# Optimization experiments

Measured on AMD Instinct MI355X. Metric: run time of the kernel, lower is better.

The kernel has to match this reference:

```python
import jax, jax.numpy as jnp
import numpy as np
from itertools import product

N = 120000      # active voxels
D = 128         # dense grid resolution per axis
CIN = 64
COUT = 64
K = 27          # 3x3x3 kernel volume
EPS = 1e-5


def setup_inputs() -> dict:
    # Build a random sparse voxel set and its kernel-offset neighbor map (torchsparse kmap).
    rng = np.random.default_rng(0)
    flat = rng.choice(D ** 3, size=N, replace=False)
    cz, cy, cx = np.unravel_index(flat, (D, D, D))
    coords = np.stack([cz, cy, cx], axis=1)               # [N, 3]
    lut = np.full(D ** 3, -1, dtype=np.int64)
    lut[flat] = np.arange(N)
    nbr = np.empty((K, N), dtype=np.int32)
    for k, (dz, dy, dx) in enumerate(product((-1, 0, 1), repeat=3)):
        nc = coords + np.array([dz, dy, dx])
        valid = np.all((nc >= 0) & (nc < D), axis=1)
        fl = np.ravel_multi_index(np.clip(nc, 0, D - 1).T, (D, D, D))
        nbr[k] = np.where(valid, lut[fl], -1).astype(np.int32)

    key = jax.random.key(0)
    k1, k2, k3, k4 = jax.random.split(key, 4)
    feats = jax.random.normal(k1, (N, CIN), dtype=jnp.float32)
    # torchsparse Conv3d weight layout: [kernel_volume, in_channels, out_channels]
    weight = jax.random.normal(k2, (K, CIN, COUT), dtype=jnp.float32) / np.float32(np.sqrt(K * CIN))
    gamma = jax.random.uniform(k3, (COUT,), dtype=jnp.float32, minval=0.5, maxval=1.5)
    beta = jax.random.normal(k4, (COUT,), dtype=jnp.float32) * 0.1
    return {"feats": feats, "weight": weight, "gamma": gamma, "beta": beta,
            "neighbor_idx": jnp.asarray(nbr)}


def reference(feats, weight, gamma, beta, neighbor_idx):
    # Sparse conv = gather -> per-offset matmul -> accumulate (stride 1, same voxel set).
    mask = (neighbor_idx >= 0)                      # [K, N]
    safe = jnp.maximum(neighbor_idx, 0)
    gathered = feats[safe] * mask[..., None]        # [K, N, Cin], missing neighbors zeroed
    out = jnp.einsum('knc,kcd->nd', gathered, weight)  # [N, Cout]
    # BatchNorm over active voxels (training-mode batch statistics), then ReLU.
    mean = out.mean(axis=0)
    var = out.var(axis=0)
    y = gamma * (out - mean) * jax.lax.rsqrt(var + EPS) + beta
    return jnp.maximum(y, 0.0)
```

## Files before the change

### kernel.cpp

```cpp
#include <hip/hip_runtime.h>

#define NVOX 120000
#define KVOL 27
#define CH 64
#define TOTAL (NVOX * CH)
#define NF4 (TOTAL / 4)
#define EPSV 1e-5f

typedef __attribute__((ext_vector_type(8))) short bf16x8;
typedef __attribute__((ext_vector_type(8))) unsigned short u16x8;
typedef __attribute__((ext_vector_type(4))) float f32x4;
typedef __attribute__((address_space(1))) const void gconst_t;
typedef __attribute__((address_space(3))) void lvoid_t;

__device__ __forceinline__ unsigned short f2bf(float f) {
    unsigned int u = __builtin_bit_cast(unsigned int, f);
    u += 0x7FFFu + ((u >> 16) & 1u);
    return (unsigned short)(u >> 16);
}

#define PGRID (27 + 3750)
__global__ void prep(const float* __restrict__ w, const float* __restrict__ feats,
                     unsigned short* __restrict__ wtf, unsigned short* __restrict__ fb,
                     float* __restrict__ stats) {
    __shared__ unsigned short ls[4096];
    const int b = blockIdx.x;
    const int tid = threadIdx.x;
    if (b < KVOL) {
        const int k = b;
        float4 v[4];
        const float4* src = (const float4*)(w + (size_t)k * 4096 + tid * 16);
#pragma unroll
        for (int i = 0; i < 4; ++i) v[i] = src[i];
#pragma unroll
        for (int e = 0; e < 16; ++e) {
            const int t = tid * 16 + e;
            const int d = t & 63, c = t >> 6;
            const int grp = (d >> 4) * 2 + (c >> 5);
            const int l = ((c & 31) >> 3) * 16 + (d & 15);
            const int j = c & 7;
            ls[(grp * 64 + l) * 8 + j] = f2bf(((const float*)v)[e]);
        }
        __syncthreads();
        u16x8* dst = (u16x8*)(wtf + (size_t)k * 4096);
        const u16x8* lsv = (const u16x8*)ls;
        dst[tid * 2]     = lsv[tid * 2];
        dst[tid * 2 + 1] = lsv[tid * 2 + 1];
        if (b == 0 && tid < 128) stats[tid] = 0.f;
        if (b == 1 && tid < 8) ((u16x8*)fb)[(size_t)NVOX * 8 + tid] = (u16x8)0;
    } else {
        const int t = (b - KVOL) * 256 + tid;
        const float4* src = (const float4*)feats + (size_t)t * 2;
        const float4 p0 = src[0];
        const float4 p1 = src[1];
        u16x8 v = {f2bf(p0.x), f2bf(p0.y), f2bf(p0.z), f2bf(p0.w),
                   f2bf(p1.x), f2bf(p1.y), f2bf(p1.z), f2bf(p1.w)};
        ((u16x8*)fb)[t] = v;
    }
}

__launch_bounds__(256, 4)
__global__ void conv_mfma(const unsigned short* __restrict__ FB,
                          const unsigned short* __restrict__ WtF,
                          const int* __restrict__ nbr,
                          float* __restrict__ out,
                          float* __restrict__ stats) {
    __shared__ unsigned short wlds[2][4096];
    __shared__ float lstats[128];
    const int tid = threadIdx.x;
    const int lane = tid & 63;
    const int wv = tid >> 6;
    const int m = lane & 15;
    const int q = lane >> 4;
    const int v0 = blockIdx.x * 128 + wv * 32;
    const bool tv[2] = { v0 < NVOX, v0 + 16 < NVOX };
    const int r[2] = { v0 + m, v0 + 16 + m };

    f32x4 acc[2][4];
#pragma unroll
    for (int t = 0; t < 2; ++t)
#pragma unroll
        for (int nt = 0; nt < 4; ++nt)
            acc[t][nt] = (f32x4){0.f, 0.f, 0.f, 0.f};
    if (tid < 128) lstats[tid] = 0.f;

    const bf16x8* fbv = (const bf16x8*)FB;

    {
        const unsigned short* g = WtF + wv * 1024 + lane * 8;
        __builtin_amdgcn_global_load_lds((gconst_t*)g,         (lvoid_t*)&wlds[0][wv * 1024],       16, 0, 0);
        __builtin_amdgcn_global_load_lds((gconst_t*)(g + 512), (lvoid_t*)&wlds[0][wv * 1024 + 512], 16, 0, 0);
    }
    __builtin_amdgcn_sched_barrier(0);

    bf16x8 a[2][2];
    unsigned long long msk[2];
    int idxn[2];
#pragma unroll
    for (int t = 0; t < 2; ++t) {
        const int rr = tv[t] ? r[t] : m;
        const int i0 = nbr[rr];
        const int i = tv[t] ? i0 : -1;
        msk[t] = __ballot(i >= 0);
        const bf16x8* row = fbv + (size_t)(i < 0 ? NVOX : i) * 8;
        a[t][0] = row[q];
        a[t][1] = row[q + 4];
        const int i1 = nbr[NVOX + rr];
        idxn[t] = tv[t] ? i1 : -1;
    }
    asm volatile("s_waitcnt vmcnt(6) lgkmcnt(0)" ::: "memory");
    __builtin_amdgcn_s_barrier();
    __builtin_amdgcn_sched_barrier(0);

    for (int k = 0; k < KVOL; ++k) {
        const int nb = k & 1;
        if (k + 1 < KVOL) {
            const unsigned short* g = WtF + (size_t)(k + 1) * 4096 + wv * 1024 + lane * 8;
            __builtin_amdgcn_global_load_lds((gconst_t*)g,         (lvoid_t*)&wlds[nb ^ 1][wv * 1024],       16, 0, 0);
            __builtin_amdgcn_global_load_lds((gconst_t*)(g + 512), (lvoid_t*)&wlds[nb ^ 1][wv * 1024 + 512], 16, 0, 0);
        }
        __builtin_amdgcn_sched_barrier(0);

        unsigned long long mn[2];
        bf16x8 an[2][2];
#pragma unroll
        for (int t = 0; t < 2; ++t) {
            mn[t] = __ballot(idxn[t] >= 0);
            const bf16x8* rw = fbv + (size_t)(idxn[t] < 0 ? NVOX : idxn[t]) * 8;
            an[t][0] = rw[q];
            an[t][1] = rw[q + 4];
        }
        const int kk = (k + 2 < KVOL) ? (k + 2) : 0;
        const int* nbp = nbr + (size_t)kk * NVOX;
        int idxf[2];
#pragma unroll
        for (int t = 0; t < 2; ++t) {
            const int rr = tv[t] ? r[t] : m;
            const int v = nbp[rr];
            idxf[t] = (tv[t] && (k + 2 < KVOL)) ? v : -1;
        }

        const unsigned short* wk = &wlds[nb][lane * 8];
        bf16x8 bfr[8];
#pragma unroll
        for (int h = 0; h < 8; ++h)
            bfr[h] = *(const bf16x8*)(wk + h * 512);

#pragma unroll
        for (int t = 0; t < 2; ++t) {
            if (msk[t]) {
#pragma unroll
                for (int nt = 0; nt < 4; ++nt) {
                    acc[t][nt] = __builtin_amdgcn_mfma_f32_16x16x32_bf16(a[t][0], bfr[nt * 2 + 0], acc[t][nt], 0, 0, 0);
                    acc[t][nt] = __builtin_amdgcn_mfma_f32_16x16x32_bf16(a[t][1], bfr[nt * 2 + 1], acc[t][nt], 0, 0, 0);
                }
            }
        }

#pragma unroll
        for (int t = 0; t < 2; ++t) {
            a[t][0] = an[t][0];
            a[t][1] = an[t][1];
            msk[t] = mn[t];
            idxn[t] = idxf[t];
        }

        asm volatile("s_waitcnt vmcnt(6)" ::: "memory");
        __builtin_amdgcn_s_barrier();
        __builtin_amdgcn_sched_barrier(0);
    }

#pragma unroll
    for (int t = 0; t < 2; ++t) {
        if (tv[t]) {
            float* ob = out + (size_t)(v0 + t * 16 + q * 4) * CH + m;
#pragma unroll
            for (int nt = 0; nt < 4; ++nt)
#pragma unroll
                for (int rr = 0; rr < 4; ++rr)
                    ob[(size_t)rr * CH + nt * 16] = acc[t][nt][rr];
        }
    }

#pragma unroll
    for (int nt = 0; nt < 4; ++nt) {
        float s = 0.f, s2 = 0.f;
#pragma unroll
        for (int t = 0; t < 2; ++t)
#pragma unroll
            for (int rr = 0; rr < 4; ++rr) {
                const float x = acc[t][nt][rr];
                s += x;
                s2 = fmaf(x, x, s2);
            }
        s  += __shfl_xor(s, 16);  s  += __shfl_xor(s, 32);
        s2 += __shfl_xor(s2, 16); s2 += __shfl_xor(s2, 32);
        if (lane < 16) {
            atomicAdd(&lstats[nt * 16 + m], s);
            atomicAdd(&lstats[64 + nt * 16 + m], s2);
        }
    }
    __syncthreads();
    if (tid < 128) atomicAdd(&stats[tid], lstats[tid]);
}

__launch_bounds__(256)
__global__ void bn_relu(float* __restrict__ out, const float* __restrict__ stats,
                        const float* __restrict__ gamma, const float* __restrict__ beta) {
    __shared__ float sb[128];
    const int tid = threadIdx.x;
    if (tid < 64) {
        const float inv_n = 1.0f / (float)NVOX;
        const float mean = stats[tid] * inv_n;
        const float var = stats[64 + tid] * inv_n - mean * mean;
        const float sc = gamma[tid] * rsqrtf(var + EPSV);
        sb[tid] = sc;
        sb[64 + tid] = beta[tid] - mean * sc;
    }
    __syncthreads();
    float4* o4 = (float4*)out;
    const int base = blockIdx.x * 256 + tid;
    const int cb = (base & 15) * 4;
    const float s0 = sb[cb + 0], s1 = sb[cb + 1], s2 = sb[cb + 2], s3 = sb[cb + 3];
    const float b0 = sb[64 + cb + 0], b1 = sb[64 + cb + 1], b2 = sb[64 + cb + 2], b3 = sb[64 + cb + 3];
#pragma unroll
    for (int i = 0; i < 4; ++i) {
        const int e = base + i * 480000;
        float4 x = o4[e];
        x.x = fmaxf(fmaf(x.x, s0, b0), 0.f);
        x.y = fmaxf(fmaf(x.y, s1, b1), 0.f);
        x.z = fmaxf(fmaf(x.z, s2, b2), 0.f);
        x.w = fmaxf(fmaf(x.w, s3, b3), 0.f);
        o4[e] = x;
    }
}

extern "C" void kernel_launch(void* const* d_in, const int* in_sizes, int n_in,
                              void* d_out, int out_size, void* d_ws, size_t ws_size,
                              hipStream_t stream) {
    const float* feats  = (const float*)d_in[0];
    const float* weight = (const float*)d_in[1];
    const float* gamma  = (const float*)d_in[2];
    const float* beta   = (const float*)d_in[3];
    const int*   nbr    = (const int*)d_in[4];
    float* out = (float*)d_out;

    float* stats = (float*)d_ws;
    unsigned short* WtF = (unsigned short*)((char*)d_ws + 512);
    unsigned short* FB  = (unsigned short*)((char*)d_ws + 512 + 221184);

    prep<<<PGRID, 256, 0, stream>>>(weight, feats, WtF, FB, stats);
    conv_mfma<<<(NVOX + 127) / 128, 256, 0, stream>>>(FB, WtF, nbr, out, stats);
    bn_relu<<<1875, 256, 0, stream>>>(out, stats, gamma, beta);
}
```

Before: 154.2 us.

## Load weight fragments directly into registers and drop LDS staging and barriers

Weight fragments are no longer staged through double-buffered LDS with global_load_lds and per-offset block barriers. Each wave now reads its B fragments straight from global memory into registers, ping-ponging two register sets across a two-way unrolled loop. This removes the LDS traffic and block-wide synchronisation from the main loop. In exchange every wave issues its own weight loads, which should hit in L2, and register pressure rises, so launch bounds drop from 4 to 3 blocks per CU. A __syncthreads is added before the LDS stats reduction.

New measurement: 162.2 us. 5.2% more time.

```diff
diff --git a/kernel.cpp b/kernel.cpp
--- a/kernel.cpp
+++ b/kernel.cpp
@@ -10,8 +10,6 @@
 typedef __attribute__((ext_vector_type(8))) short bf16x8;
 typedef __attribute__((ext_vector_type(8))) unsigned short u16x8;
 typedef __attribute__((ext_vector_type(4))) float f32x4;
-typedef __attribute__((address_space(1))) const void gconst_t;
-typedef __attribute__((address_space(3))) void lvoid_t;
 
 __device__ __forceinline__ unsigned short f2bf(float f) {
     unsigned int u = __builtin_bit_cast(unsigned int, f);
@@ -59,13 +57,12 @@
     }
 }
 
-__launch_bounds__(256, 4)
+__launch_bounds__(256, 3)
 __global__ void conv_mfma(const unsigned short* __restrict__ FB,
                           const unsigned short* __restrict__ WtF,
                           const int* __restrict__ nbr,
                           float* __restrict__ out,
                           float* __restrict__ stats) {
-    __shared__ unsigned short wlds[2][4096];
     __shared__ float lstats[128];
     const int tid = threadIdx.x;
     const int lane = tid & 63;
@@ -85,89 +82,74 @@
     if (tid < 128) lstats[tid] = 0.f;
 
     const bf16x8* fbv = (const bf16x8*)FB;
-
-    {
-        const unsigned short* g = WtF + wv * 1024 + lane * 8;
-        __builtin_amdgcn_global_load_lds((gconst_t*)g,         (lvoid_t*)&wlds[0][wv * 1024],       16, 0, 0);
-        __builtin_amdgcn_global_load_lds((gconst_t*)(g + 512), (lvoid_t*)&wlds[0][wv * 1024 + 512], 16, 0, 0);
-    }
-    __builtin_amdgcn_sched_barrier(0);
-
-    bf16x8 a[2][2];
-    unsigned long long msk[2];
-    int idxn[2];
+    const bf16x8* wfr = (const bf16x8*)WtF + lane;
+
+    bf16x8 bfrA[8], bfrB[8];
+#pragma unroll
+    for (int h = 0; h < 8; ++h) bfrA[h] = wfr[h * 64];
+
+    bf16x8 aA[2][2], aB[2][2];
+    bool mskA[2], mskB[2];
+    int ixA[2], ixB[2];
 #pragma unroll
     for (int t = 0; t < 2; ++t) {
         const int rr = tv[t] ? r[t] : m;
         const int i0 = nbr[rr];
         const int i = tv[t] ? i0 : -1;
-        msk[t] = __ballot(i >= 0);
+        mskA[t] = (__ballot(i >= 0) != 0ULL);
         const bf16x8* row = fbv + (size_t)(i < 0 ? NVOX : i) * 8;
-        a[t][0] = row[q];
-        a[t][1] = row[q + 4];
+        aA[t][0] = row[q];
+        aA[t][1] = row[q + 4];
         const int i1 = nbr[NVOX + rr];
-        idxn[t] = tv[t] ? i1 : -1;
-    }
-    asm volatile("s_waitcnt vmcnt(6) lgkmcnt(0)" ::: "memory");
-    __builtin_amdgcn_s_barrier();
-    __builtin_amdgcn_sched_barrier(0);
-
-    for (int k = 0; k < KVOL; ++k) {
-        const int nb = k & 1;
-        if (k + 1 < KVOL) {
-            const unsigned short* g = WtF + (size_t)(k + 1) * 4096 + wv * 1024 + lane * 8;
-            __builtin_amdgcn_global_load_lds((gconst_t*)g,         (lvoid_t*)&wlds[nb ^ 1][wv * 1024],       16, 0, 0);
-            __builtin_amdgcn_global_load_lds((gconst_t*)(g + 512), (lvoid_t*)&wlds[nb ^ 1][wv * 1024 + 512], 16, 0, 0);
-        }
-        __builtin_amdgcn_sched_barrier(0);
-
-        unsigned long long mn[2];
-        bf16x8 an[2][2];
+        ixA[t] = tv[t] ? i1 : -1;
+    }
+
+    auto phase = [&](const bf16x8 (&bfrC)[8], bf16x8 (&bfrN)[8],
+                     const bf16x8 (&aC)[2][2], bf16x8 (&aN)[2][2],
+                     const bool (&mC)[2], bool (&mN)[2],
+                     const int (&ixC)[2], int (&ixN)[2], const int k) {
+#pragma unroll
+        for (int h = 0; h < 8; ++h) bfrN[h] = wfr[(k + 1) * 512 + h * 64];
 #pragma unroll
         for (int t = 0; t < 2; ++t) {
-            mn[t] = __ballot(idxn[t] >= 0);
-            const bf16x8* rw = fbv + (size_t)(idxn[t] < 0 ? NVOX : idxn[t]) * 8;
-            an[t][0] = rw[q];
-            an[t][1] = rw[q + 4];
+            mN[t] = (__ballot(ixC[t] >= 0) != 0ULL);
+            const bf16x8* rw = fbv + (size_t)(ixC[t] < 0 ? NVOX : ixC[t]) * 8;
+            aN[t][0] = rw[q];
+            aN[t][1] = rw[q + 4];
         }
         const int kk = (k + 2 < KVOL) ? (k + 2) : 0;
         const int* nbp = nbr + (size_t)kk * NVOX;
-        int idxf[2];
 #pragma unroll
         for (int t = 0; t < 2; ++t) {
             const int rr = tv[t] ? r[t] : m;
             const int v = nbp[rr];
-            idxf[t] = (tv[t] && (k + 2 < KVOL)) ? v : -1;
-        }
-
-        const unsigned short* wk = &wlds[nb][lane * 8];
-        bf16x8 bfr[8];
-#pragma unroll
-        for (int h = 0; h < 8; ++h)
-            bfr[h] = *(const bf16x8*)(wk + h * 512);
-
+            ixN[t] = (tv[t] && (k + 2 < KVOL)) ? v : -1;
+        }
 #pragma unroll
         for (int t = 0; t < 2; ++t) {
-            if (msk[t]) {
+            if (mC[t]) {
 #pragma unroll
                 for (int nt = 0; nt < 4; ++nt) {
-                    acc[t][nt] = __builtin_amdgcn_mfma_f32_16x16x32_bf16(a[t][0], bfr[nt * 2 + 0], acc[t][nt], 0, 0, 0);
-                    acc[t][nt] = __builtin_amdgcn_mfma_f32_16x16x32_bf16(a[t][1], bfr[nt * 2 + 1], acc[t][nt], 0, 0, 0);
+                    acc[t][nt] = __builtin_amdgcn_mfma_f32_16x16x32_bf16(aC[t][0], bfrC[nt * 2 + 0], acc[t][nt], 0, 0, 0);
+                    acc[t][nt] = __builtin_amdgcn_mfma_f32_16x16x32_bf16(aC[t][1], bfrC[nt * 2 + 1], acc[t][nt], 0, 0, 0);
                 }
             }
         }
-
-#pragma unroll
-        for (int t = 0; t < 2; ++t) {
-            a[t][0] = an[t][0];
-            a[t][1] = an[t][1];
-            msk[t] = mn[t];
-            idxn[t] = idxf[t];
-        }
-
-        asm volatile("s_waitcnt vmcnt(6)" ::: "memory");
-        __builtin_amdgcn_s_barrier();
-        __builtin_amdgcn_sched_barrier(0);
+    };
+
+    for (int k = 0; k < KVOL - 1; k += 2) {
+        phase(bfrA, bfrB, aA, aB, mskA, mskB, ixA, ixB, k);
+        phase(bfrB, bfrA, aB, aA, mskB, mskA, ixB, ixA, k + 1);
+    }
+#pragma unroll
+    for (int t = 0; t < 2; ++t) {
+        if (mskA[t]) {
+#pragma unroll
+            for (int nt = 0; nt < 4; ++nt) {
+                acc[t][nt] = __builtin_amdgcn_mfma_f32_16x16x32_bf16(aA[t][0], bfrA[nt * 2 + 0], acc[t][nt], 0, 0, 0);
+                acc[t][nt] = __builtin_amdgcn_mfma_f32_16x16x32_bf16(aA[t][1], bfrA[nt * 2 + 1], acc[t][nt], 0, 0, 0);
+            }
+        }
     }
 
 #pragma unroll
@@ -182,6 +164,7 @@
         }
     }
 
+    __syncthreads();
 #pragma unroll
     for (int nt = 0; nt < 4; ++nt) {
         float s = 0.f, s2 = 0.f;
```

## Gather fp32 features directly in conv and convert to bf16 in-register

Applied to the files above, without the earlier changes.

Removes the separate feature-to-bf16 conversion pass from the prep kernel, so the conv kernel gathers fp32 rows straight from the input and converts them to bf16 in registers before the MFMAs. This saves a full read and write of the feature array plus most of the prep launch. The cost is that each gather now moves twice as many bytes per neighbor across 27 offsets, and more registers are needed. Occupancy is lowered to 3 waves, and the software pipeline is rewritten as a ping-pong double-buffered lambda with a vmcnt of 10. The skip of all-invalid MFMA groups is also dropped in favor of zeroing invalid rows.

Result: slower. 184.0 us (+19.3%).

```diff
diff --git a/kernel.cpp b/kernel.cpp
--- a/kernel.cpp
+++ b/kernel.cpp
@@ -19,48 +19,34 @@
     return (unsigned short)(u >> 16);
 }
 
-#define PGRID (27 + 3750)
-__global__ void prep(const float* __restrict__ w, const float* __restrict__ feats,
-                     unsigned short* __restrict__ wtf, unsigned short* __restrict__ fb,
+__global__ void prep(const float* __restrict__ w, unsigned short* __restrict__ wtf,
                      float* __restrict__ stats) {
     __shared__ unsigned short ls[4096];
-    const int b = blockIdx.x;
+    const int k = blockIdx.x;
     const int tid = threadIdx.x;
-    if (b < KVOL) {
-        const int k = b;
-        float4 v[4];
-        const float4* src = (const float4*)(w + (size_t)k * 4096 + tid * 16);
-#pragma unroll
-        for (int i = 0; i < 4; ++i) v[i] = src[i];
-#pragma unroll
-        for (int e = 0; e < 16; ++e) {
-            const int t = tid * 16 + e;
-            const int d = t & 63, c = t >> 6;
-            const int grp = (d >> 4) * 2 + (c >> 5);
-            const int l = ((c & 31) >> 3) * 16 + (d & 15);
-            const int j = c & 7;
-            ls[(grp * 64 + l) * 8 + j] = f2bf(((const float*)v)[e]);
-        }
-        __syncthreads();
-        u16x8* dst = (u16x8*)(wtf + (size_t)k * 4096);
-        const u16x8* lsv = (const u16x8*)ls;
-        dst[tid * 2]     = lsv[tid * 2];
-        dst[tid * 2 + 1] = lsv[tid * 2 + 1];
-        if (b == 0 && tid < 128) stats[tid] = 0.f;
-        if (b == 1 && tid < 8) ((u16x8*)fb)[(size_t)NVOX * 8 + tid] = (u16x8)0;
-    } else {
-        const int t = (b - KVOL) * 256 + tid;
-        const float4* src = (const float4*)feats + (size_t)t * 2;
-        const float4 p0 = src[0];
-        const float4 p1 = src[1];
-        u16x8 v = {f2bf(p0.x), f2bf(p0.y), f2bf(p0.z), f2bf(p0.w),
-                   f2bf(p1.x), f2bf(p1.y), f2bf(p1.z), f2bf(p1.w)};
-        ((u16x8*)fb)[t] = v;
-    }
-}
-
-__launch_bounds__(256, 4)
-__global__ void conv_mfma(const unsigned short* __restrict__ FB,
+    float4 v[4];
+    const float4* src = (const float4*)(w + (size_t)k * 4096 + tid * 16);
+#pragma unroll
+    for (int i = 0; i < 4; ++i) v[i] = src[i];
+#pragma unroll
+    for (int e = 0; e < 16; ++e) {
+        const int t = tid * 16 + e;
+        const int d = t & 63, c = t >> 6;
+        const int grp = (d >> 4) * 2 + (c >> 5);
+        const int l = ((c & 31) >> 3) * 16 + (d & 15);
+        const int j = c & 7;
+        ls[(grp * 64 + l) * 8 + j] = f2bf(((const float*)v)[e]);
+    }
+    __syncthreads();
+    u16x8* dst = (u16x8*)(wtf + (size_t)k * 4096);
+    const u16x8* lsv = (const u16x8*)ls;
+    dst[tid * 2]     = lsv[tid * 2];
+    dst[tid * 2 + 1] = lsv[tid * 2 + 1];
+    if (k == 0 && tid < 128) stats[tid] = 0.f;
+}
+
+__launch_bounds__(256, 3)
+__global__ void conv_mfma(const float* __restrict__ feats,
                           const unsigned short* __restrict__ WtF,
                           const int* __restrict__ nbr,
                           float* __restrict__ out,
@@ -84,8 +70,6 @@
             acc[t][nt] = (f32x4){0.f, 0.f, 0.f, 0.f};
     if (tid < 128) lstats[tid] = 0.f;
 
-    const bf16x8* fbv = (const bf16x8*)FB;
-
     {
         const unsigned short* g = WtF + wv * 1024 + lane * 8;
         __builtin_amdgcn_global_load_lds((gconst_t*)g,         (lvoid_t*)&wlds[0][wv * 1024],       16, 0, 0);
@@ -93,26 +77,30 @@
     }
     __builtin_amdgcn_sched_barrier(0);
 
-    bf16x8 a[2][2];
-    unsigned long long msk[2];
-    int idxn[2];
+    float4 pA[2][4], pB[2][4];
+    bool invA[2], invB[2];
+    int ixA[2], ixB[2];
 #pragma unroll
     for (int t = 0; t < 2; ++t) {
         const int rr = tv[t] ? r[t] : m;
         const int i0 = nbr[rr];
-        const int i = tv[t] ? i0 : -1;
-        msk[t] = __ballot(i >= 0);
-        const bf16x8* row = fbv + (size_t)(i < 0 ? NVOX : i) * 8;
-        a[t][0] = row[q];
-        a[t][1] = row[q + 4];
+        const int ii = tv[t] ? i0 : -1;
+        invA[t] = (ii < 0);
+        const float* row = feats + (size_t)(ii < 0 ? 0 : ii) * CH + q * 8;
+        pA[t][0] = *(const float4*)(row);
+        pA[t][1] = *(const float4*)(row + 4);
+        pA[t][2] = *(const float4*)(row + 32);
+        pA[t][3] = *(const float4*)(row + 36);
         const int i1 = nbr[NVOX + rr];
-        idxn[t] = tv[t] ? i1 : -1;
-    }
-    asm volatile("s_waitcnt vmcnt(6) lgkmcnt(0)" ::: "memory");
+        ixA[t] = tv[t] ? i1 : -1;
+    }
+    asm volatile("s_waitcnt vmcnt(10) lgkmcnt(0)" ::: "memory");
     __builtin_amdgcn_s_barrier();
     __builtin_amdgcn_sched_barrier(0);
 
-    for (int k = 0; k < KVOL; ++k) {
+    auto phase = [&](const float4 (&pC)[2][4], float4 (&pN)[2][4],
+                     const bool (&invC)[2], bool (&invN)[2],
+                     const int (&ixC)[2], int (&ixN)[2], const int k) {
         const int nb = k & 1;
         if (k + 1 < KVOL) {
             const unsigned short* g = WtF + (size_t)(k + 1) * 4096 + wv * 1024 + lane * 8;
@@ -121,23 +109,23 @@
         }
         __builtin_amdgcn_sched_barrier(0);
 
-        unsigned long long mn[2];
-        bf16x8 an[2][2];
 #pragma unroll
         for (int t = 0; t < 2; ++t) {
-            mn[t] = __ballot(idxn[t] >= 0);
-            const bf16x8* rw = fbv + (size_t)(idxn[t] < 0 ? NVOX : idxn[t]) * 8;
-            an[t][0] = rw[q];
-            an[t][1] = rw[q + 4];
+            const int ii = ixC[t];
+            invN[t] = (ii < 0);
+            const float* row = feats + (size_t)(ii < 0 ? 0 : ii) * CH + q * 8;
+            pN[t][0] = *(const float4*)(row);
+            pN[t][1] = *(const float4*)(row + 4);
+            pN[t][2] = *(const float4*)(row + 32);
+            pN[t][3] = *(const float4*)(row + 36);
         }
         const int kk = (k + 2 < KVOL) ? (k + 2) : 0;
         const int* nbp = nbr + (size_t)kk * NVOX;
-        int idxf[2];
 #pragma unroll
         for (int t = 0; t < 2; ++t) {
             const int rr = tv[t] ? r[t] : m;
             const int v = nbp[rr];
-            idxf[t] = (tv[t] && (k + 2 < KVOL)) ? v : -1;
+            ixN[t] = (tv[t] && (k + 2 < KVOL)) ? v : -1;
         }
 
         const unsigned short* wk = &wlds[nb][lane * 8];
@@ -148,27 +136,32 @@
 
 #pragma unroll
         for (int t = 0; t < 2; ++t) {
-            if (msk[t]) {
-#pragma unroll
-                for (int nt = 0; nt < 4; ++nt) {
-                    acc[t][nt] = __builtin_amdgcn_mfma_f32_16x16x32_bf16(a[t][0], bfr[nt * 2 + 0], acc[t][nt], 0, 0, 0);
-                    acc[t][nt] = __builtin_amdgcn_mfma_f32_16x16x32_bf16(a[t][1], bfr[nt * 2 + 1], acc[t][nt], 0, 0, 0);
-                }
+            bf16x8 a0 = (bf16x8){(short)f2bf(pC[t][0].x), (short)f2bf(pC[t][0].y),
+                                 (short)f2bf(pC[t][0].z), (short)f2bf(pC[t][0].w),
+                                 (short)f2bf(pC[t][1].x), (short)f2bf(pC[t][1].y),
+                                 (short)f2bf(pC[t][1].z), (short)f2bf(pC[t][1].w)};
+            bf16x8 a1 = (bf16x8){(short)f2bf(pC[t][2].x), (short)f2bf(pC[t][2].y),
+                                 (short)f2bf(pC[t][2].z), (short)f2bf(pC[t][2].w),
+                                 (short)f2bf(pC[t][3].x), (short)f2bf(pC[t][3].y),
+                                 (short)f2bf(pC[t][3].z), (short)f2bf(pC[t][3].w)};
+            if (invC[t]) { a0 = (bf16x8)(short)0; a1 = (bf16x8)(short)0; }
+#pragma unroll
+            for (int nt = 0; nt < 4; ++nt) {
+                acc[t][nt] = __builtin_amdgcn_mfma_f32_16x16x32_bf16(a0, bfr[nt * 2 + 0], acc[t][nt], 0, 0, 0);
+                acc[t][nt] = __builtin_amdgcn_mfma_f32_16x16x32_bf16(a1, bfr[nt * 2 + 1], acc[t][nt], 0, 0, 0);
             }
         }
 
-#pragma unroll
-        for (int t = 0; t < 2; ++t) {
-            a[t][0] = an[t][0];
-            a[t][1] = an[t][1];
-            msk[t] = mn[t];
-            idxn[t] = idxf[t];
-        }
-
-        asm volatile("s_waitcnt vmcnt(6)" ::: "memory");
+        asm volatile("s_waitcnt vmcnt(10)" ::: "memory");
         __builtin_amdgcn_s_barrier();
         __builtin_amdgcn_sched_barrier(0);
-    }
+    };
+
+    for (int k = 0; k < KVOL - 1; k += 2) {
+        phase(pA, pB, invA, invB, ixA, ixB, k);
+        phase(pB, pA, invB, invA, ixB, ixA, k + 1);
+    }
+    phase(pA, pB, invA, invB, ixA, ixB, KVOL - 1);
 
 #pragma unroll
     for (int t = 0; t < 2; ++t) {
@@ -247,9 +240,8 @@
 
     float* stats = (float*)d_ws;
     unsigned short* WtF = (unsigned short*)((char*)d_ws + 512);
-    unsigned short* FB  = (unsigned short*)((char*)d_ws + 512 + 221184);
-
-    prep<<<PGRID, 256, 0, stream>>>(weight, feats, WtF, FB, stats);
-    conv_mfma<<<(NVOX + 127) / 128, 256, 0, stream>>>(FB, WtF, nbr, out, stats);
+
+    prep<<<KVOL, 256, 0, stream>>>(weight, WtF, stats);
+    conv_mfma<<<(NVOX + 127) / 128, 256, 0, stream>>>(feats, WtF, nbr, out, stats);
     bn_relu<<<1875, 256, 0, stream>>>(out, stats, gamma, beta);
 }
```
